# Performance work log

Measured on AMD Instinct MI355X. Metric: run time of the kernel, lower is better.

Reference implementation:

```python
import jax, jax.numpy as jnp
import numpy as np

E = 512
H = 8
D = E // H
HID = 2048
NE = 4
TOPK = 2
EPS = 1e-5
NEG = -1e9


def _ln(x, w, b):
    mu = jnp.mean(x, axis=-1, keepdims=True)
    var = jnp.mean(jnp.square(x - mu), axis=-1, keepdims=True)
    return (x - mu) * jax.lax.rsqrt(var + EPS) * w + b


def _expert(xf, mask, ln1_w, ln1_b, ipw, ipb, opw, opb, ln2_w, ln2_b, w1, b1, w2, b2):
    # xf: [T, E]; mask: [T] bool (allowed keys = routed tokens)
    T = xf.shape[0]
    h = _ln(xf, ln1_w, ln1_b)
    qkv = h @ ipw.T + ipb                       # [T, 3E]
    q, k, v = jnp.split(qkv, 3, axis=-1)
    q = q.reshape(T, H, D).transpose(1, 0, 2)   # [H, T, D]
    k = k.reshape(T, H, D).transpose(1, 0, 2)
    v = v.reshape(T, H, D).transpose(1, 0, 2)
    scores = jnp.einsum('htd,hsd->hts', q, k) / jnp.sqrt(jnp.asarray(D, xf.dtype))
    scores = jnp.where(mask[None, None, :], scores, NEG)
    a = jax.nn.softmax(scores, axis=-1)
    o = jnp.einsum('hts,hsd->htd', a, v).transpose(1, 0, 2).reshape(T, E)
    o = o @ opw.T + opb
    x1 = xf + o                                 # residual (dropout = identity, eval)
    h2 = _ln(x1, ln2_w, ln2_b)
    m = jax.nn.gelu(h2 @ w1.T + b1, approximate=False) @ w2.T + b2
    return x1 + m


def setup_inputs() -> dict:
    key = jax.random.key(0)
    ks = jax.random.split(key, 16)
    s = 0.02
    inp = {
        'x': jax.random.normal(ks[0], (4, 512, E), dtype=jnp.float32),
        'gate_w': jax.random.normal(ks[1], (NE, E), dtype=jnp.float32) * s,
        'gate_b': jnp.zeros((NE,), jnp.float32),
        'ln1_w': jnp.ones((NE, E), jnp.float32),
        'ln1_b': jnp.zeros((NE, E), jnp.float32),
        'in_proj_w': jax.random.normal(ks[2], (NE, 3 * E, E), dtype=jnp.float32) * s,
        'in_proj_b': jnp.zeros((NE, 3 * E), jnp.float32),
        'out_proj_w': jax.random.normal(ks[3], (NE, E, E), dtype=jnp.float32) * s,
        'out_proj_b': jnp.zeros((NE, E), jnp.float32),
        'ln2_w': jnp.ones((NE, E), jnp.float32),
        'ln2_b': jnp.zeros((NE, E), jnp.float32),
        'mlp_w1': jax.random.normal(ks[4], (NE, HID, E), dtype=jnp.float32) * s,
        'mlp_b1': jnp.zeros((NE, HID), jnp.float32),
        'mlp_w2': jax.random.normal(ks[5], (NE, E, HID), dtype=jnp.float32) * s,
        'mlp_b2': jnp.zeros((NE, E), jnp.float32),
    }
    return inp


def reference(x, gate_w, gate_b, ln1_w, ln1_b, in_proj_w, in_proj_b, out_proj_w,
              out_proj_b, ln2_w, ln2_b, mlp_w1, mlp_b1, mlp_w2, mlp_b2):
    B, N, _ = x.shape
    T = B * N
    xf = x.reshape(T, E)
    logits = xf @ gate_w.T + gate_b                      # [T, NE]
    topk_val, topk_idx = jax.lax.top_k(logits, TOPK)
    probs = jax.nn.softmax(topk_val, axis=-1)            # [T, TOPK]
    out = jnp.zeros_like(xf)
    for kk in range(TOPK):
        idx = topk_idx[:, kk]
        w = probs[:, kk][:, None]
        for e in range(NE):
            mask = idx == e
            eo = _expert(xf, mask,
                         ln1_w[e], ln1_b[e], in_proj_w[e], in_proj_b[e],
                         out_proj_w[e], out_proj_b[e], ln2_w[e], ln2_b[e],
                         mlp_w1[e], mlp_b1[e], mlp_w2[e], mlp_b2[e])
            out = out + jnp.where(mask[:, None], eo * w, 0.0)
    return out.reshape(B, N, E)
```

## Files before the change

kernel.cpp:

```cpp
#include <hip/hip_runtime.h>
#include <hip/hip_bf16.h>

#define T_TOK 2048
#define E_DIM 512
#define NHEAD 8
#define DHEAD 64
#define HID_D 2048
#define NEXP 4
#define NROW_ (2 * T_TOK)
#define VT_STRIDE 4608

typedef short short8 __attribute__((ext_vector_type(8)));
typedef float floatx4 __attribute__((ext_vector_type(4)));

__device__ __forceinline__ void gld16(const void* g, void* l) {
  __builtin_amdgcn_global_load_lds((const __attribute__((address_space(1))) void*)g,
                                   (__attribute__((address_space(3))) void*)l, 16, 0, 0);
}

__device__ inline float wave_sum(float v) {
  for (int off = 32; off > 0; off >>= 1) v += __shfl_xor(v, off);
  return v;
}

__device__ __forceinline__ unsigned pack_bf2(float a, float b) {
  __hip_bfloat16 ha = __float2bfloat16(a), hb = __float2bfloat16(b);
  unsigned ua = *(unsigned short*)&ha, ub = *(unsigned short*)&hb;
  return ua | (ub << 16);
}

__device__ __forceinline__ void cvt4(const float* __restrict__ s, __hip_bfloat16* __restrict__ d,
                                     int i4, int n) {
  if (i4 < n) {
    float4 v = *reinterpret_cast<const float4*>(s + i4);
    __hip_bfloat16 tmp[4] = {__float2bfloat16(v.x), __float2bfloat16(v.y),
                             __float2bfloat16(v.z), __float2bfloat16(v.w)};
    *reinterpret_cast<ushort4*>(d + i4) = *reinterpret_cast<const ushort4*>(tmp);
  }
}

__global__ void cvt_weights(const float* __restrict__ s0, const float* __restrict__ s1,
                            const float* __restrict__ s2, const float* __restrict__ s3,
                            __hip_bfloat16* d0, __hip_bfloat16* d1,
                            __hip_bfloat16* d2, __hip_bfloat16* d3,
                            int n0, int n1, int n2, int n3) {
  int i4 = (blockIdx.x * 256 + threadIdx.x) * 4;
  cvt4(s0, d0, i4, n0);
  cvt4(s1, d1, i4, n1);
  cvt4(s2, d2, i4, n2);
  cvt4(s3, d3, i4, n3);
}

__global__ void gate_kernel(const float* __restrict__ x, const float* __restrict__ gw,
                            const float* __restrict__ gb, int* token_e, float* token_p) {
  int wid = threadIdx.x >> 6, lane = threadIdx.x & 63;
  int t = blockIdx.x * 4 + wid;
  float a0 = 0, a1 = 0, a2 = 0, a3 = 0;
  for (int i = 0; i < 8; i++) {
    int c = lane + 64 * i;
    float xv = x[(size_t)t * E_DIM + c];
    a0 += xv * gw[0 * E_DIM + c];
    a1 += xv * gw[1 * E_DIM + c];
    a2 += xv * gw[2 * E_DIM + c];
    a3 += xv * gw[3 * E_DIM + c];
  }
  a0 = wave_sum(a0); a1 = wave_sum(a1); a2 = wave_sum(a2); a3 = wave_sum(a3);
  if (lane == 0) {
    float lg[4] = {a0 + gb[0], a1 + gb[1], a2 + gb[2], a3 + gb[3]};
    int i0 = 0;
    for (int e = 1; e < 4; e++) if (lg[e] > lg[i0]) i0 = e;
    int i1 = -1;
    for (int e = 0; e < 4; e++) {
      if (e == i0) continue;
      if (i1 < 0 || lg[e] > lg[i1]) i1 = e;
    }
    float e1 = __expf(lg[i1] - lg[i0]);
    float inv = 1.f / (1.f + e1);
    token_e[t] = i0; token_e[T_TOK + t] = i1;
    token_p[t] = inv; token_p[T_TOK + t] = e1 * inv;
  }
}

__global__ void route_kernel(const int* __restrict__ token_e, int* perm, int* rowg,
                             int* pmap, int* invrow, int* offs_out, int* padoffs_out) {
  int g = blockIdx.x, kk = g >> 2, e = g & 3;
  int tid = threadIdx.x, wid = tid >> 6, lane = tid & 63;
  __shared__ int cnt_s[8][4];
  for (int gg = 0; gg < 8; gg++) {
    int kk2 = gg >> 2, e2 = gg & 3;
    int c = 0;
    for (int t = tid; t < T_TOK; t += 256) c += (token_e[kk2 * T_TOK + t] == e2);
    for (int off = 32; off; off >>= 1) c += __shfl_xor(c, off);
    if (lane == 0) cnt_s[gg][wid] = c;
  }
  __syncthreads();
  int offs[9], padoffs[9];
  offs[0] = 0; padoffs[0] = 0;
  for (int gg = 0; gg < 8; gg++) {
    int c = cnt_s[gg][0] + cnt_s[gg][1] + cnt_s[gg][2] + cnt_s[gg][3];
    offs[gg + 1] = offs[gg] + c;
    padoffs[gg + 1] = padoffs[gg] + ((c + 63) & ~63);
  }
  if (g == 0 && tid < 9) { offs_out[tid] = offs[tid]; padoffs_out[tid] = padoffs[tid]; }
  int og = offs[g], pg = padoffs[g];
  __shared__ int wcnt[4];
  __shared__ int base;
  if (tid == 0) base = 0;
  __syncthreads();
  for (int t0 = 0; t0 < T_TOK; t0 += 256) {
    int t = t0 + tid;
    bool pred = token_e[kk * T_TOK + t] == e;
    unsigned long long mask = __ballot(pred);
    int rank = __popcll(mask & ((1ull << lane) - 1ull));
    if (lane == 0) wcnt[wid] = __popcll(mask);
    __syncthreads();
    int woff = 0;
    for (int i = 0; i < wid; i++) woff += wcnt[i];
    if (pred) {
      int row = og + base + woff + rank;
      perm[row] = t;
      rowg[row] = g;
      pmap[row] = pg + (row - og);
      invrow[kk * T_TOK + t] = row;
    }
    __syncthreads();
    if (tid == 0) base += wcnt[0] + wcnt[1] + wcnt[2] + wcnt[3];
    __syncthreads();
  }
}

__global__ void ln_kernel(const float* __restrict__ src, const int* __restrict__ perm,
                          const int* __restrict__ rowg, const float* __restrict__ lnw,
                          const float* __restrict__ lnb, __hip_bfloat16* __restrict__ dst) {
  int wid = threadIdx.x >> 6, lane = threadIdx.x & 63;
  int row = blockIdx.x * 4 + wid;
  int e = rowg[row] & 3;
  const float* xr = src + (size_t)(perm ? perm[row] : row) * E_DIM;
  float v[8];
  float s = 0;
  for (int i = 0; i < 8; i++) { v[i] = xr[lane + 64 * i]; s += v[i]; }
  s = wave_sum(s);
  float mu = s * (1.f / 512.f);
  float q = 0;
  for (int i = 0; i < 8; i++) { float d = v[i] - mu; q += d * d; }
  q = wave_sum(q);
  float rstd = rsqrtf(q * (1.f / 512.f) + 1e-5f);
  for (int i = 0; i < 8; i++) {
    int c = lane + 64 * i;
    dst[(size_t)row * E_DIM + c] =
        __float2bfloat16((v[i] - mu) * rstd * lnw[e * E_DIM + c] + lnb[e * E_DIM + c]);
  }
}

__global__ void transpose_v(const short* __restrict__ v, const int* __restrict__ pmap,
                            short* __restrict__ vT) {
  __shared__ short tile[64][65];
  int r0 = blockIdx.x * 64, c0 = blockIdx.y * 64;
  int tc = threadIdx.x & 63, tr4 = threadIdx.x >> 6;
  for (int i = 0; i < 64; i += 4)
    tile[tr4 + i][tc] = v[(size_t)(r0 + tr4 + i) * E_DIM + c0 + tc];
  __syncthreads();
  int pcol = pmap[r0 + tc];
  for (int i = 0; i < 64; i += 4)
    vT[(size_t)(c0 + tr4 + i) * VT_STRIDE + pcol] = tile[tc][tr4 + i];
}

__global__ void zero_gaps(const int* __restrict__ offs, const int* __restrict__ padoffs,
                          short* __restrict__ vT) {
  int g = blockIdx.x;
  int cnt = offs[g + 1] - offs[g];
  int gap = (padoffs[g + 1] - padoffs[g]) - cnt;
  if ((int)threadIdx.x < gap) {
    int col = padoffs[g] + cnt + threadIdx.x;
    for (int d = blockIdx.y; d < E_DIM; d += gridDim.y)
      vT[(size_t)d * VT_STRIDE + col] = 0;
  }
}

__global__ __launch_bounds__(256) void attn_mfma(
    const short* __restrict__ qb, const short* __restrict__ kb,
    const short* __restrict__ vT, const int* __restrict__ offs,
    const int* __restrict__ padoffs, __hip_bfloat16* __restrict__ ob) {
  int d0 = blockIdx.x;
  int g = d0 & 7;
  int rem = d0 >> 3;
  int h = rem >> 5;
  int qblk = rem & 31;
  int sbeg = offs[g], rend = offs[g + 1];
  int q0 = sbeg + qblk * 64;
  if (q0 >= rend) return;
  int G = rend - sbeg;
  int pg = padoffs[g];
  int tid = threadIdx.x, wid = tid >> 6, lane = tid & 63;
  int fr = lane & 15, lg = lane >> 4;
  int qw = q0 + wid * 16;

  __shared__ short Kt[3][64 * 64];
  __shared__ short Vt[3][64 * 64];

  int arow = qw + fr; if (arow > rend - 1) arow = rend - 1;
  const short* qp = qb + (size_t)arow * E_DIM + h * DHEAD;
  short8 qf0 = *reinterpret_cast<const short8*>(qp + lg * 8);
  short8 qf1 = *reinterpret_cast<const short8*>(qp + 32 + lg * 8);

  int st_row[2], st_src[2];
  int wb = wid << 9;
  for (int c = 0; c < 2; c++) {
    int off = c * 4096 + tid * 16;
    int row = off >> 7, inner = off & 127;
    st_row[c] = row;
    st_src[c] = (inner ^ ((row & 7) << 4)) >> 1;
  }

  auto stage = [&](int buf, int kbase) {
#pragma unroll
    for (int c = 0; c < 2; c++) {
      int gr = sbeg + kbase + st_row[c]; if (gr > NROW_ - 1) gr = NROW_ - 1;
      gld16(kb + (size_t)gr * E_DIM + h * DHEAD + st_src[c], &Kt[buf][c * 2048 + wb]);
      gld16(vT + (size_t)(h * DHEAD + st_row[c]) * VT_STRIDE + pg + kbase + st_src[c],
            &Vt[buf][c * 2048 + wb]);
    }
  };

  floatx4 acc[4] = {};
  float m_r = -1e30f, l_r = 0.f;
  int nt = (G + 63) >> 6;

  stage(0, 0);
  if (nt > 1) stage(1, 64);
  if (nt > 1) asm volatile("s_waitcnt vmcnt(4)" ::: "memory");
  else        asm volatile("s_waitcnt vmcnt(0)" ::: "memory");
  __builtin_amdgcn_s_barrier();
  __builtin_amdgcn_sched_barrier(0);

  int bcur = 0;
  for (int t = 0; t < nt; ++t) {
    int kbase = t * 64;
    int b2 = bcur + 2; if (b2 >= 3) b2 -= 3;
    if (t + 2 < nt) stage(b2, kbase + 128);
    const char* Kb = (const char*)&Kt[bcur][0];
    const char* Vb = (const char*)&Vt[bcur][0];

    floatx4 s[4];
    __builtin_amdgcn_s_setprio(1);
#pragma unroll
    for (int c = 0; c < 4; c++) {
      int rc = c * 16 + fr;
      int sx = (rc & 7) << 4;
      short8 kf0 = *reinterpret_cast<const short8*>(Kb + rc * 128 + ((lg * 16) ^ sx));
      short8 kf1 = *reinterpret_cast<const short8*>(Kb + rc * 128 + ((64 + lg * 16) ^ sx));
      floatx4 z = {};
      z = __builtin_amdgcn_mfma_f32_16x16x32_bf16(kf0, qf0, z, 0, 0, 0);
      z = __builtin_amdgcn_mfma_f32_16x16x32_bf16(kf1, qf1, z, 0, 0, 0);
      s[c] = z;
    }
    __builtin_amdgcn_s_setprio(0);

    float sv[16];
    float mloc = -1e30f;
#pragma unroll
    for (int c = 0; c < 4; c++)
#pragma unroll
      for (int j = 0; j < 4; j++) {
        int k0 = kbase + c * 16 + lg * 4 + j;
        float v = (k0 < G) ? s[c][j] * 0.125f : -1e30f;
        sv[c * 4 + j] = v;
        mloc = fmaxf(mloc, v);
      }
    mloc = fmaxf(mloc, __shfl_xor(mloc, 16));
    mloc = fmaxf(mloc, __shfl_xor(mloc, 32));
    if (__any(mloc > m_r + 8.f)) {
      float mn = fmaxf(m_r, mloc);
      float corr = __expf(m_r - mn);
      m_r = mn;
      l_r *= corr;
      float cq0 = __shfl(corr, lg * 4 + 0), cq1 = __shfl(corr, lg * 4 + 1);
      float cq2 = __shfl(corr, lg * 4 + 2), cq3 = __shfl(corr, lg * 4 + 3);
#pragma unroll
      for (int db = 0; db < 4; db++) {
        acc[db][0] *= cq0; acc[db][1] *= cq1; acc[db][2] *= cq2; acc[db][3] *= cq3;
      }
    }
    float p[16], sl = 0.f;
#pragma unroll
    for (int i = 0; i < 16; i++) { p[i] = __expf(sv[i] - m_r); sl += p[i]; }
    sl += __shfl_xor(sl, 16);
    sl += __shfl_xor(sl, 32);
    l_r += sl;

    union { unsigned u[4]; short8 s8; } pa[4];
#pragma unroll
    for (int c = 0; c < 4; c++) {
      pa[c].u[0] = pack_bf2(p[c * 4 + 0], p[c * 4 + 1]);
      pa[c].u[1] = pack_bf2(p[c * 4 + 2], p[c * 4 + 3]);
      pa[c].u[2] = 0; pa[c].u[3] = 0;
    }
    __builtin_amdgcn_s_setprio(1);
#pragma unroll
    for (int db = 0; db < 4; db++) {
      int dd = db * 16 + fr;
      int sx = (dd & 7) << 4;
#pragma unroll
      for (int c = 0; c < 4; c++) {
        uint2 w = *reinterpret_cast<const uint2*>(Vb + ((dd * 128 + c * 32 + lg * 8) ^ sx));
        union { unsigned u[4]; short8 s8; } bv;
        bv.u[0] = w.x; bv.u[1] = w.y; bv.u[2] = 0; bv.u[3] = 0;
        acc[db] = __builtin_amdgcn_mfma_f32_16x16x32_bf16(pa[c].s8, bv.s8, acc[db], 0, 0, 0);
      }
    }
    __builtin_amdgcn_s_setprio(0);

    if (t + 1 < nt) {
      if (t + 2 < nt) asm volatile("s_waitcnt vmcnt(4)" ::: "memory");
      else            asm volatile("s_waitcnt vmcnt(0)" ::: "memory");
      asm volatile("s_waitcnt lgkmcnt(0)" ::: "memory");
      __builtin_amdgcn_s_barrier();
      __builtin_amdgcn_sched_barrier(0);
    }
    bcur = bcur + 1; if (bcur == 3) bcur = 0;
  }

  float lq0 = __shfl(l_r, lg * 4 + 0), lq1 = __shfl(l_r, lg * 4 + 1);
  float lq2 = __shfl(l_r, lg * 4 + 2), lq3 = __shfl(l_r, lg * 4 + 3);
  float lq[4] = {lq0, lq1, lq2, lq3};
#pragma unroll
  for (int db = 0; db < 4; db++)
#pragma unroll
    for (int j = 0; j < 4; j++) {
      int row = qw + lg * 4 + j;
      if (row < rend)
        ob[(size_t)row * E_DIM + h * DHEAD + db * 16 + fr] = __float2bfloat16(acc[db][j] / lq[j]);
    }
}

template <int MODE>
__global__ __launch_bounds__(256) void gemm_mfma(
    const short* __restrict__ A, const short* __restrict__ Wb,
    const float* __restrict__ bias, const int* __restrict__ offs,
    const int* __restrict__ perm, const float* __restrict__ resid,
    __hip_bfloat16* __restrict__ bq, __hip_bfloat16* __restrict__ bk,
    __hip_bfloat16* __restrict__ bv, float* __restrict__ outf,
    float* __restrict__ outf2) {
  constexpr int K = (MODE == 3) ? HID_D : E_DIM;
  constexpr int N = (MODE == 0) ? 3 * E_DIM : (MODE == 2) ? HID_D : E_DIM;
  constexpr bool SPLIT = (MODE == 3);
  constexpr int KLEN = SPLIT ? K / 2 : K;
  constexpr int NKSTEP = KLEN / 64;
  constexpr int NXB = 32;
  __shared__ short Abuf[3][4096];
  __shared__ short Bbuf[3][4096];

  int d = blockIdx.x;
  int g = d & 7;
  int rem = d >> 3;
  int ksel = 0;
  if constexpr (SPLIT) { ksel = rem & 1; rem >>= 1; }
  int yb = rem / NXB, xb = rem % NXB;
  int e = g & 3;
  int rbeg = offs[g], rend = offs[g + 1];
  int row0 = rbeg + xb * 64;
  if (row0 >= rend) return;
  int col0 = yb * 64;
  int kbeg = ksel * KLEN;
  int tid = threadIdx.x;
  int wid = tid >> 6, lane = tid & 63;
  int wm = wid >> 1, wn = wid & 1;
  int fr = lane & 15, lg = lane >> 4;
  const short* wbase = Wb + (size_t)e * N * K;

  int st_row[2], st_src[2], st_arow[2];
  int wavebase = wid << 9;
  for (int c = 0; c < 2; c++) {
    int off = c * 4096 + tid * 16;
    int trow = off >> 7;
    int inner = off & 127;
    st_row[c] = trow;
    st_src[c] = (inner ^ ((trow & 7) << 4)) >> 1;
    int ga = row0 + trow;
    st_arow[c] = ga < rend ? ga : rend - 1;
  }

  auto stage = [&](int buf, int kb) {
#pragma unroll
    for (int c = 0; c < 2; c++) {
      gld16(A + (size_t)st_arow[c] * K + kb + st_src[c], &Abuf[buf][c * 2048 + wavebase]);
      gld16(wbase + (size_t)(col0 + st_row[c]) * K + kb + st_src[c],
            &Bbuf[buf][c * 2048 + wavebase]);
    }
  };

  floatx4 acc[2][2] = {};
  stage(0, kbeg);
  stage(1, kbeg + 64);
  asm volatile("s_waitcnt vmcnt(4)" ::: "memory");
  __builtin_amdgcn_s_barrier();
  __builtin_amdgcn_sched_barrier(0);

  int bcur = 0;
  for (int t = 0; t < NKSTEP; ++t) {
    int b2 = bcur + 2; if (b2 >= 3) b2 -= 3;
    if (t + 2 < NKSTEP) stage(b2, kbeg + (t + 2) * 64);
    const char* Ab = (const char*)&Abuf[bcur][0];
    const char* Bb = (const char*)&Bbuf[bcur][0];
    short8 af[2][2], bf8[2][2];
#pragma unroll
    for (int mi = 0; mi < 2; mi++)
#pragma unroll
      for (int ks = 0; ks < 2; ks++) {
        int row = wm * 32 + mi * 16 + fr;
        int cb = ks * 64 + lg * 16;
        af[mi][ks] = *reinterpret_cast<const short8*>(Ab + row * 128 + (cb ^ ((row & 7) << 4)));
      }
#pragma unroll
    for (int ni = 0; ni < 2; ni++)
#pragma unroll
      for (int ks = 0; ks < 2; ks++) {
        int row = wn * 32 + ni * 16 + fr;
        int cb = ks * 64 + lg * 16;
        bf8[ni][ks] = *reinterpret_cast<const short8*>(Bb + row * 128 + (cb ^ ((row & 7) << 4)));
      }
#pragma unroll
    for (int mi = 0; mi < 2; mi++)
#pragma unroll
      for (int ni = 0; ni < 2; ni++) {
        acc[mi][ni] = __builtin_amdgcn_mfma_f32_16x16x32_bf16(af[mi][0], bf8[ni][0], acc[mi][ni], 0, 0, 0);
        acc[mi][ni] = __builtin_amdgcn_mfma_f32_16x16x32_bf16(af[mi][1], bf8[ni][1], acc[mi][ni], 0, 0, 0);
      }
    if (t + 1 < NKSTEP) {
      if (t + 2 < NKSTEP) asm volatile("s_waitcnt vmcnt(4)" ::: "memory");
      else                asm volatile("s_waitcnt vmcnt(0)" ::: "memory");
      asm volatile("s_waitcnt lgkmcnt(0)" ::: "memory");
      __builtin_amdgcn_s_barrier();
      __builtin_amdgcn_sched_barrier(0);
    }
    bcur = (bcur + 1 == 3) ? 0 : bcur + 1;
  }

  for (int mi = 0; mi < 2; mi++)
    for (int ni = 0; ni < 2; ni++)
      for (int j = 0; j < 4; j++) {
        int row = row0 + wm * 32 + mi * 16 + lg * 4 + j;
        if (row >= rend) continue;
        int col = col0 + wn * 32 + ni * 16 + fr;
        float val = acc[mi][ni][j];
        if constexpr (MODE != 3) val += bias[e * N + col];
        if constexpr (MODE == 0) {
          if (col < E_DIM) bq[(size_t)row * E_DIM + col] = __float2bfloat16(val);
          else if (col < 2 * E_DIM) bk[(size_t)row * E_DIM + col - E_DIM] = __float2bfloat16(val);
          else bv[(size_t)row * E_DIM + col - 2 * E_DIM] = __float2bfloat16(val);
        } else if constexpr (MODE == 1) {
          int t = perm[row];
          outf[(size_t)row * E_DIM + col] = val + resid[(size_t)t * E_DIM + col];
        } else if constexpr (MODE == 2) {
          float gl = 0.5f * val * (1.f + erff(val * 0.70710678118654752f));
          bq[(size_t)row * HID_D + col] = __float2bfloat16(gl);
        } else {
          if (ksel == 0) {
            val += bias[e * N + col] + resid[(size_t)row * E_DIM + col];
            outf[(size_t)row * E_DIM + col] = val;
          } else {
            outf2[(size_t)row * E_DIM + col] = val;
          }
        }
      }
}

__global__ void combine_kernel(const float* __restrict__ y1, const float* __restrict__ y2,
                               const int* __restrict__ invrow,
                               const float* __restrict__ token_p, float* __restrict__ out) {
  int t = blockIdx.x;
  int r0 = invrow[t], r1 = invrow[T_TOK + t];
  float p0 = token_p[t], p1 = token_p[T_TOK + t];
  const float4* a0 = (const float4*)(y1 + (size_t)r0 * E_DIM);
  const float4* b0 = (const float4*)(y2 + (size_t)r0 * E_DIM);
  const float4* a1 = (const float4*)(y1 + (size_t)r1 * E_DIM);
  const float4* b1 = (const float4*)(y2 + (size_t)r1 * E_DIM);
  float4* o = (float4*)(out + (size_t)t * E_DIM);
  int i = threadIdx.x;
  float4 va0 = a0[i], vb0 = b0[i], va1 = a1[i], vb1 = b1[i];
  float4 r;
  r.x = p0 * (va0.x + vb0.x) + p1 * (va1.x + vb1.x);
  r.y = p0 * (va0.y + vb0.y) + p1 * (va1.y + vb1.y);
  r.z = p0 * (va0.z + vb0.z) + p1 * (va1.z + vb1.z);
  r.w = p0 * (va0.w + vb0.w) + p1 * (va1.w + vb1.w);
  o[i] = r;
}

extern "C" void kernel_launch(void* const* d_in, const int* in_sizes, int n_in,
                              void* d_out, int out_size, void* d_ws, size_t ws_size,
                              hipStream_t stream) {
  const float* x      = (const float*)d_in[0];
  const float* gate_w = (const float*)d_in[1];
  const float* gate_b = (const float*)d_in[2];
  const float* ln1_w  = (const float*)d_in[3];
  const float* ln1_b  = (const float*)d_in[4];
  const float* ipw    = (const float*)d_in[5];
  const float* ipb    = (const float*)d_in[6];
  const float* opw    = (const float*)d_in[7];
  const float* opb    = (const float*)d_in[8];
  const float* ln2_w  = (const float*)d_in[9];
  const float* ln2_b  = (const float*)d_in[10];
  const float* w1     = (const float*)d_in[11];
  const float* b1     = (const float*)d_in[12];
  const float* w2     = (const float*)d_in[13];
  const float* b2     = (const float*)d_in[14];
  float* out = (float*)d_out;

  const int SZ_IP = NEXP * 3 * E_DIM * E_DIM;
  const int SZ_OP = NEXP * E_DIM * E_DIM;
  const int SZ_W1 = NEXP * HID_D * E_DIM;
  const int SZ_W2 = NEXP * E_DIM * HID_D;
  const int NROW = NROW_;

  char* ws = (char*)d_ws;
  size_t off = 0;
  auto carve = [&](size_t bytes) -> void* {
    void* p = ws + off;
    off += (bytes + 255) & ~(size_t)255;
    return p;
  };
  __hip_bfloat16* ipw_bf = (__hip_bfloat16*)carve((size_t)SZ_IP * 2);
  __hip_bfloat16* opw_bf = (__hip_bfloat16*)carve((size_t)SZ_OP * 2);
  __hip_bfloat16* w1_bf  = (__hip_bfloat16*)carve((size_t)SZ_W1 * 2);
  __hip_bfloat16* w2_bf  = (__hip_bfloat16*)carve((size_t)SZ_W2 * 2);
  __hip_bfloat16* h_bf   = (__hip_bfloat16*)carve((size_t)NROW * E_DIM * 2);
  __hip_bfloat16* q_bf   = (__hip_bfloat16*)carve((size_t)NROW * E_DIM * 2);
  __hip_bfloat16* k_bf   = (__hip_bfloat16*)carve((size_t)NROW * E_DIM * 2);
  __hip_bfloat16* v_bf   = (__hip_bfloat16*)carve((size_t)NROW * E_DIM * 2);
  __hip_bfloat16* o_bf   = (__hip_bfloat16*)carve((size_t)NROW * E_DIM * 2);
  __hip_bfloat16* h2_bf  = (__hip_bfloat16*)carve((size_t)NROW * E_DIM * 2);
  __hip_bfloat16* mid_bf = (__hip_bfloat16*)carve((size_t)NROW * HID_D * 2);
  short* vT     = (short*)carve((size_t)E_DIM * VT_STRIDE * 2);
  float* x1     = (float*)carve((size_t)NROW * E_DIM * 4);
  int* token_e  = (int*)carve((size_t)NROW * 4);
  float* token_p= (float*)carve((size_t)NROW * 4);
  int* perm     = (int*)carve((size_t)NROW * 4);
  int* rowg     = (int*)carve((size_t)NROW * 4);
  int* pmap     = (int*)carve((size_t)NROW * 4);
  int* invrow   = (int*)carve((size_t)NROW * 4);
  int* offs     = (int*)carve(9 * 4);
  int* padoffs  = (int*)carve(9 * 4);
  float* ybuf  = (float*)h_bf;
  float* ybuf2 = (float*)k_bf;

  cvt_weights<<<SZ_W1 / 4 / 256, 256, 0, stream>>>(ipw, opw, w1, w2, ipw_bf, opw_bf,
                                                   w1_bf, w2_bf, SZ_IP, SZ_OP, SZ_W1, SZ_W2);
  gate_kernel<<<T_TOK / 4, 256, 0, stream>>>(x, gate_w, gate_b, token_e, token_p);
  route_kernel<<<8, 256, 0, stream>>>(token_e, perm, rowg, pmap, invrow, offs, padoffs);
  ln_kernel<<<NROW / 4, 256, 0, stream>>>(x, perm, rowg, ln1_w, ln1_b, h_bf);
  gemm_mfma<0><<<8 * 24 * 32, 256, 0, stream>>>((const short*)h_bf, (const short*)ipw_bf,
      ipb, offs, perm, nullptr, q_bf, k_bf, v_bf, nullptr, nullptr);
  transpose_v<<<dim3(NROW / 64, E_DIM / 64), 256, 0, stream>>>((const short*)v_bf, pmap, vT);
  zero_gaps<<<dim3(8, 64), 64, 0, stream>>>(offs, padoffs, vT);
  attn_mfma<<<8 * 8 * 32, 256, 0, stream>>>((const short*)q_bf, (const short*)k_bf,
      vT, offs, padoffs, o_bf);
  gemm_mfma<1><<<8 * 8 * 32, 256, 0, stream>>>((const short*)o_bf, (const short*)opw_bf,
      opb, offs, perm, x, nullptr, nullptr, nullptr, x1, nullptr);
  ln_kernel<<<NROW / 4, 256, 0, stream>>>(x1, nullptr, rowg, ln2_w, ln2_b, h2_bf);
  gemm_mfma<2><<<8 * 32 * 32, 256, 0, stream>>>((const short*)h2_bf, (const short*)w1_bf,
      b1, offs, perm, nullptr, mid_bf, nullptr, nullptr, nullptr, nullptr);
  gemm_mfma<3><<<8 * 2 * 8 * 32, 256, 0, stream>>>((const short*)mid_bf, (const short*)w2_bf,
      b2, offs, perm, x1, nullptr, nullptr, nullptr, ybuf, ybuf2);
  combine_kernel<<<T_TOK, 128, 0, stream>>>(ybuf, ybuf2, invrow, token_p, out);
  (void)in_sizes; (void)n_in; (void)ws_size;
}
```

Before: 176.3 us.

## Load attention K/V fragments directly from global and fuse gap zeroing into transpose

The attention kernel drops its triple-buffered LDS staging of K and V tiles, along with the waitcnt and barrier synchronisation that went with it. Each lane now reads its K and V^T MFMA fragments straight from global memory, relying on L2/L1 caching to serve the reuse across the block's four waves. The separate zero_gaps launch is folded into transpose_v, which removes one kernel launch. The risk is that every wave now issues redundant global loads without prefetch, and the fused zeroing could race with the transpose writes if the padded columns overlap.

```diff
diff --git a/kernel.cpp b/kernel.cpp
--- a/kernel.cpp
+++ b/kernel.cpp
@@ -153,6 +153,7 @@
 }
 
 __global__ void transpose_v(const short* __restrict__ v, const int* __restrict__ pmap,
+                            const int* __restrict__ offs, const int* __restrict__ padoffs,
                             short* __restrict__ vT) {
   __shared__ short tile[64][65];
   int r0 = blockIdx.x * 64, c0 = blockIdx.y * 64;
@@ -163,17 +164,17 @@
   int pcol = pmap[r0 + tc];
   for (int i = 0; i < 64; i += 4)
     vT[(size_t)(c0 + tr4 + i) * VT_STRIDE + pcol] = tile[tc][tr4 + i];
-}
-
-__global__ void zero_gaps(const int* __restrict__ offs, const int* __restrict__ padoffs,
-                          short* __restrict__ vT) {
-  int g = blockIdx.x;
-  int cnt = offs[g + 1] - offs[g];
-  int gap = (padoffs[g + 1] - padoffs[g]) - cnt;
-  if ((int)threadIdx.x < gap) {
-    int col = padoffs[g] + cnt + threadIdx.x;
-    for (int d = blockIdx.y; d < E_DIM; d += gridDim.y)
-      vT[(size_t)d * VT_STRIDE + col] = 0;
+  int gg = blockIdx.x;
+  if (gg < 8) {
+    int cnt = offs[gg + 1] - offs[gg];
+    int gap = (padoffs[gg + 1] - padoffs[gg]) - cnt;
+    int colbase = padoffs[gg] + cnt;
+    if (gap > 0) {
+      for (int dl = 0; dl < 64; dl += 4) {
+        int d = c0 + dl + tr4;
+        if (tc < gap) vT[(size_t)d * VT_STRIDE + colbase + tc] = 0;
+      }
+    }
   }
 }
 
@@ -195,60 +196,30 @@
   int fr = lane & 15, lg = lane >> 4;
   int qw = q0 + wid * 16;
 
-  __shared__ short Kt[3][64 * 64];
-  __shared__ short Vt[3][64 * 64];
-
   int arow = qw + fr; if (arow > rend - 1) arow = rend - 1;
   const short* qp = qb + (size_t)arow * E_DIM + h * DHEAD;
   short8 qf0 = *reinterpret_cast<const short8*>(qp + lg * 8);
   short8 qf1 = *reinterpret_cast<const short8*>(qp + 32 + lg * 8);
 
-  int st_row[2], st_src[2];
-  int wb = wid << 9;
-  for (int c = 0; c < 2; c++) {
-    int off = c * 4096 + tid * 16;
-    int row = off >> 7, inner = off & 127;
-    st_row[c] = row;
-    st_src[c] = (inner ^ ((row & 7) << 4)) >> 1;
-  }
-
-  auto stage = [&](int buf, int kbase) {
-#pragma unroll
-    for (int c = 0; c < 2; c++) {
-      int gr = sbeg + kbase + st_row[c]; if (gr > NROW_ - 1) gr = NROW_ - 1;
-      gld16(kb + (size_t)gr * E_DIM + h * DHEAD + st_src[c], &Kt[buf][c * 2048 + wb]);
-      gld16(vT + (size_t)(h * DHEAD + st_row[c]) * VT_STRIDE + pg + kbase + st_src[c],
-            &Vt[buf][c * 2048 + wb]);
-    }
-  };
+  const short* kbh = kb + h * DHEAD + lg * 8;
+  const short* vbase = vT + (size_t)(h * DHEAD) * VT_STRIDE + pg;
 
   floatx4 acc[4] = {};
   float m_r = -1e30f, l_r = 0.f;
   int nt = (G + 63) >> 6;
 
-  stage(0, 0);
-  if (nt > 1) stage(1, 64);
-  if (nt > 1) asm volatile("s_waitcnt vmcnt(4)" ::: "memory");
-  else        asm volatile("s_waitcnt vmcnt(0)" ::: "memory");
-  __builtin_amdgcn_s_barrier();
-  __builtin_amdgcn_sched_barrier(0);
-
-  int bcur = 0;
   for (int t = 0; t < nt; ++t) {
     int kbase = t * 64;
-    int b2 = bcur + 2; if (b2 >= 3) b2 -= 3;
-    if (t + 2 < nt) stage(b2, kbase + 128);
-    const char* Kb = (const char*)&Kt[bcur][0];
-    const char* Vb = (const char*)&Vt[bcur][0];
 
     floatx4 s[4];
     __builtin_amdgcn_s_setprio(1);
 #pragma unroll
     for (int c = 0; c < 4; c++) {
-      int rc = c * 16 + fr;
-      int sx = (rc & 7) << 4;
-      short8 kf0 = *reinterpret_cast<const short8*>(Kb + rc * 128 + ((lg * 16) ^ sx));
-      short8 kf1 = *reinterpret_cast<const short8*>(Kb + rc * 128 + ((64 + lg * 16) ^ sx));
+      int krow = sbeg + kbase + c * 16 + fr;
+      if (krow > NROW_ - 1) krow = NROW_ - 1;
+      const short* kp = kbh + (size_t)krow * E_DIM;
+      short8 kf0 = *reinterpret_cast<const short8*>(kp);
+      short8 kf1 = *reinterpret_cast<const short8*>(kp + 32);
       floatx4 z = {};
       z = __builtin_amdgcn_mfma_f32_16x16x32_bf16(kf0, qf0, z, 0, 0, 0);
       z = __builtin_amdgcn_mfma_f32_16x16x32_bf16(kf1, qf1, z, 0, 0, 0);
@@ -299,25 +270,16 @@
 #pragma unroll
     for (int db = 0; db < 4; db++) {
       int dd = db * 16 + fr;
-      int sx = (dd & 7) << 4;
+      const short* vp = vbase + (size_t)dd * VT_STRIDE + kbase + lg * 4;
 #pragma unroll
       for (int c = 0; c < 4; c++) {
-        uint2 w = *reinterpret_cast<const uint2*>(Vb + ((dd * 128 + c * 32 + lg * 8) ^ sx));
+        uint2 w = *reinterpret_cast<const uint2*>(vp + c * 16);
         union { unsigned u[4]; short8 s8; } bv;
         bv.u[0] = w.x; bv.u[1] = w.y; bv.u[2] = 0; bv.u[3] = 0;
         acc[db] = __builtin_amdgcn_mfma_f32_16x16x32_bf16(pa[c].s8, bv.s8, acc[db], 0, 0, 0);
       }
     }
     __builtin_amdgcn_s_setprio(0);
-
-    if (t + 1 < nt) {
-      if (t + 2 < nt) asm volatile("s_waitcnt vmcnt(4)" ::: "memory");
-      else            asm volatile("s_waitcnt vmcnt(0)" ::: "memory");
-      asm volatile("s_waitcnt lgkmcnt(0)" ::: "memory");
-      __builtin_amdgcn_s_barrier();
-      __builtin_amdgcn_sched_barrier(0);
-    }
-    bcur = bcur + 1; if (bcur == 3) bcur = 0;
   }
 
   float lq0 = __shfl(l_r, lg * 4 + 0), lq1 = __shfl(l_r, lg * 4 + 1);
@@ -550,8 +512,8 @@
   ln_kernel<<<NROW / 4, 256, 0, stream>>>(x, perm, rowg, ln1_w, ln1_b, h_bf);
   gemm_mfma<0><<<8 * 24 * 32, 256, 0, stream>>>((const short*)h_bf, (const short*)ipw_bf,
       ipb, offs, perm, nullptr, q_bf, k_bf, v_bf, nullptr, nullptr);
-  transpose_v<<<dim3(NROW / 64, E_DIM / 64), 256, 0, stream>>>((const short*)v_bf, pmap, vT);
-  zero_gaps<<<dim3(8, 64), 64, 0, stream>>>(offs, padoffs, vT);
+  transpose_v<<<dim3(NROW / 64, E_DIM / 64), 256, 0, stream>>>((const short*)v_bf, pmap,
+      offs, padoffs, vT);
   attn_mfma<<<8 * 8 * 32, 256, 0, stream>>>((const short*)q_bf, (const short*)k_bf,
       vT, offs, padoffs, o_bf);
   gemm_mfma<1><<<8 * 8 * 32, 256, 0, stream>>>((const short*)o_bf, (const short*)opw_bf,
```

Result: slower. 248.7 us (+41.1%).
